# Kernel tuning notes

Hardware: AMD Instinct MI355X
Metric: run time of the kernel (lower is better)

The kernel has to match this reference:

```python
import jax, jax.numpy as jnp
import numpy as np

E = 1024   # embed_dim
H = 16     # num_heads
D = E // H # head dim = 64
L = 1024   # query seq len
S = 1024   # key seq len
N = 4      # batch


def _xavier(key, shape):
    fan_in, fan_out = shape[-1], shape[0]
    if len(shape) == 3:  # attn_W [D, D, H]: torch xavier treats dims (d0, d1*h)
        fan_out, fan_in = shape[0], shape[1] * shape[2]
    scale = jnp.sqrt(6.0 / (fan_in + fan_out)).astype(jnp.float32)
    return jax.random.uniform(key, shape, jnp.float32, -scale, scale)


def setup_inputs() -> dict:
    key = jax.random.key(0)
    ks = jax.random.split(key, 8)
    return {
        "Q": jax.random.normal(ks[0], (L, N, E), jnp.float32),
        "K": jax.random.normal(ks[1], (S, N, E), jnp.float32),
        "V": jax.random.normal(ks[2], (S, N, E), jnp.float32),
        "q_w": _xavier(ks[3], (E, E)),
        "k_w": _xavier(ks[4], (E, E)),
        "v_w": _xavier(ks[5], (E, E)),
        "out_w": _xavier(ks[6], (E, E)),
        "in_bias": jnp.zeros((3, E), jnp.float32),
        "out_bias": jnp.zeros((E,), jnp.float32),
        "attn_W": _xavier(ks[7], (D, D, H)),
    }


def reference(Q, K, V, q_w, k_w, v_w, out_w, in_bias, out_bias, attn_W):
    # in-projections: [l,n,e] x [o,e] -> [l,n,o]
    Qp = jnp.einsum('lni,oi->lno', Q, q_w) + in_bias[0]
    Kp = jnp.einsum('sni,oi->sno', K, k_w) + in_bias[1]
    Vp = jnp.einsum('sni,oi->sno', V, v_w) + in_bias[2]
    # split heads as (head_dim D, num_heads H) -- matches torch .view order
    Qh = Qp.reshape(L, N, D, H)
    Kh = Kp.reshape(S, N, D, H)
    Vh = Vp.reshape(S, N, D, H)
    # 'product' attention: per-head bilinear form q^T W_k k
    scores = jnp.einsum('lnok,oik,snik->lsnk', Qh, attn_W, Kh) / jnp.sqrt(jnp.float32(E))
    W = jax.nn.softmax(scores, axis=1)          # softmax over key dim s
    # dropout p=0.0 -> identity
    O = jnp.einsum('lsnk,snik->lnik', W, Vh).reshape(L, N, E)
    out = O @ out_w + out_bias
    # attention map: sum over heads, reshape [L,S,N] -> [N,L,S] (torch .view semantics = reshape)
    Wmap = W.sum(axis=-1).reshape(-1, L, S) / H
    return out, Wmap
```

## Files before the change

kernel.cpp:

```cpp
#include <hip/hip_runtime.h>
#include <cstdint>

typedef __bf16 bf16x8 __attribute__((ext_vector_type(8)));
typedef float f32x4 __attribute__((ext_vector_type(4)));

static const size_t OFF_QW2BF = 0;
static const size_t OFF_KWBF  = 524288;
static const size_t OFF_VWBF  = 1048576;
static const size_t OFF_OWTBF = 1572864;
static const size_t OFF_QB2   = 2097152;
static const size_t OFF_QWBF  = 2098176;
static const size_t OFF_KHBF  = 4195328;
static const size_t OFF_VTBF  = 6292480;
static const size_t OFF_ST    = 8389632;
static const size_t OFF_OBF   = 8520704;

__device__ inline unsigned short f2bf(float f) {
  union { float f; unsigned u; } v; v.f = f;
  const unsigned r = v.u + 0x7FFFu + ((v.u >> 16) & 1u);
  return (unsigned short)(r >> 16);
}

__global__ __launch_bounds__(256) void k_qw2(const float* __restrict__ qw,
    const float* __restrict__ attnW, const float* __restrict__ bias0,
    unsigned short* __restrict__ qw2, float* __restrict__ qb2) {
  const int b = blockIdx.x;
  const int k = b >> 6, i = b & 63;
  const int tid = threadIdx.x;
  __shared__ float aw[64];
  if (tid < 64) aw[tid] = attnW[(tid * 64 + i) * 16 + k] * 0.03125f;
  __syncthreads();
  for (int j = tid; j < 1024; j += 256) {
    float acc = 0.f;
#pragma unroll 8
    for (int o = 0; o < 64; ++o) acc = fmaf(qw[(o * 16 + k) * 1024 + j], aw[o], acc);
    qw2[(size_t)b * 1024 + j] = f2bf(acc);
  }
  if (tid == 0) {
    float acc = 0.f;
    for (int o = 0; o < 64; ++o) acc = fmaf(bias0[o * 16 + k], aw[o], acc);
    qb2[b] = acc;
  }
}

__global__ __launch_bounds__(256) void k_cvt2(const float* __restrict__ a,
    const float* __restrict__ b, unsigned short* __restrict__ oa,
    unsigned short* __restrict__ ob) {
  const int i = blockIdx.x * 256 + threadIdx.x;
  const float4 va = ((const float4*)a)[i];
  ushort4 ha; ha.x = f2bf(va.x); ha.y = f2bf(va.y); ha.z = f2bf(va.z); ha.w = f2bf(va.w);
  ((ushort4*)oa)[i] = ha;
  const float4 vb = ((const float4*)b)[i];
  ushort4 hb; hb.x = f2bf(vb.x); hb.y = f2bf(vb.y); hb.z = f2bf(vb.z); hb.w = f2bf(vb.w);
  ((ushort4*)ob)[i] = hb;
}

__global__ __launch_bounds__(256) void k_tr(const float* __restrict__ w,
    unsigned short* __restrict__ wt) {
  __shared__ float t[64][65];
  const int j0 = blockIdx.y * 64, o0 = blockIdx.x * 64;
  const int tid = threadIdx.x;
  const int r = tid >> 4, c4 = tid & 15;
#pragma unroll
  for (int q = 0; q < 4; ++q) {
    const int row = r + q * 16;
    const float4 v = *(const float4*)&w[(size_t)(j0 + row) * 1024 + o0 + c4 * 4];
    t[row][c4 * 4 + 0] = v.x; t[row][c4 * 4 + 1] = v.y;
    t[row][c4 * 4 + 2] = v.z; t[row][c4 * 4 + 3] = v.w;
  }
  __syncthreads();
#pragma unroll
  for (int q = 0; q < 4; ++q) {
    const int orow = r + q * 16;
    ushort4 h;
    h.x = f2bf(t[c4 * 4 + 0][orow]); h.y = f2bf(t[c4 * 4 + 1][orow]);
    h.z = f2bf(t[c4 * 4 + 2][orow]); h.w = f2bf(t[c4 * 4 + 3][orow]);
    *(ushort4*)&wt[(size_t)(o0 + orow) * 1024 + j0 + c4 * 4] = h;
  }
}

__global__ __launch_bounds__(256) void k_gemm_in(
    const float* __restrict__ Qf, const float* __restrict__ Kf,
    const float* __restrict__ Vf, const unsigned short* __restrict__ Bq,
    const unsigned short* __restrict__ Bk, const unsigned short* __restrict__ Bv,
    const float* __restrict__ bq, const float* __restrict__ bk,
    const float* __restrict__ bv, unsigned short* __restrict__ Cq,
    unsigned short* __restrict__ Ck, unsigned short* __restrict__ Cv) {
  __shared__ unsigned short As[128][40];
  __shared__ unsigned short Bs[128][40];
  const int id = blockIdx.x;
  const int g  = (id & 7) + ((id >> 6) << 3);
  const int bx = (id >> 3) & 7;
  const int by = g & 31, bz = g >> 5;
  const float* A          = bz == 0 ? Qf : (bz == 1 ? Kf : Vf);
  const unsigned short* B = bz == 0 ? Bq : (bz == 1 ? Bk : Bv);
  const float* bias       = bz == 0 ? bq : (bz == 1 ? bk : bv);
  unsigned short* C       = bz == 0 ? Cq : (bz == 1 ? Ck : Cv);
  const int m0 = by * 128, o0 = bx * 128;
  const int tid = threadIdx.x;
  const int wid = tid >> 6, lane = tid & 63;
  const int wr = wid >> 1, wc = wid & 1;
  const int lr = lane & 15, lk = lane >> 4;
  f32x4 acc[4][4];
#pragma unroll
  for (int i = 0; i < 4; ++i)
#pragma unroll
    for (int j = 0; j < 4; ++j) acc[i][j] = (f32x4){0.f, 0.f, 0.f, 0.f};

  for (int k0 = 0; k0 < 1024; k0 += 32) {
#pragma unroll
    for (int q = 0; q < 4; ++q) {
      const int idx = tid + q * 256;
      const int row = idx >> 3, c4 = idx & 7;
      const float4 v = *(const float4*)&A[(size_t)(m0 + row) * 1024 + k0 + c4 * 4];
      ushort4 h; h.x = f2bf(v.x); h.y = f2bf(v.y); h.z = f2bf(v.z); h.w = f2bf(v.w);
      *(ushort4*)&As[row][c4 * 4] = h;
    }
#pragma unroll
    for (int q = 0; q < 2; ++q) {
      const int idx = tid + q * 256;
      const int row = idx >> 2, c8 = idx & 3;
      *(int4*)&Bs[row][c8 * 8] =
          *(const int4*)&B[(size_t)(o0 + row) * 1024 + k0 + c8 * 8];
    }
    __syncthreads();
    bf16x8 af[4], bfr[4];
#pragma unroll
    for (int f = 0; f < 4; ++f)
      af[f] = *(const bf16x8*)&As[wr * 64 + f * 16 + lr][lk * 8];
#pragma unroll
    for (int f = 0; f < 4; ++f)
      bfr[f] = *(const bf16x8*)&Bs[wc * 64 + f * 16 + lr][lk * 8];
#pragma unroll
    for (int i = 0; i < 4; ++i)
#pragma unroll
      for (int j = 0; j < 4; ++j)
        acc[i][j] = __builtin_amdgcn_mfma_f32_16x16x32_bf16(af[i], bfr[j], acc[i][j], 0, 0, 0);
    __syncthreads();
  }
#pragma unroll
  for (int fi = 0; fi < 4; ++fi)
#pragma unroll
    for (int fj = 0; fj < 4; ++fj) {
      const int o = o0 + wc * 64 + fj * 16 + lr;
      const float bo = bias[o];
#pragma unroll
      for (int t = 0; t < 4; ++t) {
        const int m = m0 + wr * 64 + fi * 16 + lk * 4 + t;
        const float v = acc[fi][fj][t] + bo;
        const int l = m >> 2, nn = m & 3;
        if (bz == 0) {
          const int kk = o >> 6, ii = o & 63;
          C[(((size_t)(nn * 16 + kk) * 1024 + l) << 6) + ii] = f2bf(v);
        } else if (bz == 1) {
          const int kk = o & 15, ii = o >> 4;
          C[(((size_t)(nn * 16 + kk) * 1024 + l) << 6) + ii] = f2bf(v);
        } else {
          const int kk = o & 15, ii = o >> 4;
          C[(((size_t)(nn * 16 + kk) * 64 + ii) << 10) + l] = f2bf(v);
        }
      }
    }
}

__global__ __launch_bounds__(256) void k_gemm_out(
    const unsigned short* __restrict__ A, const unsigned short* __restrict__ B,
    const float* __restrict__ bias, float* __restrict__ C) {
  __shared__ unsigned short As[64][40];
  __shared__ unsigned short Bs[128][40];
  const int id = blockIdx.x;
  const int g  = (id & 7) + ((id >> 6) << 3);
  const int bx = (id >> 3) & 7;
  const int m0 = g * 64, o0 = bx * 128;
  const int tid = threadIdx.x;
  const int wid = tid >> 6, lane = tid & 63;
  const int wr = wid >> 1, wc = wid & 1;
  const int lr = lane & 15, lk = lane >> 4;
  f32x4 acc[2][4];
#pragma unroll
  for (int i = 0; i < 2; ++i)
#pragma unroll
    for (int j = 0; j < 4; ++j) acc[i][j] = (f32x4){0.f, 0.f, 0.f, 0.f};

  for (int k0 = 0; k0 < 1024; k0 += 32) {
    {
      const int row = tid >> 2, c8 = tid & 3;
      *(int4*)&As[row][c8 * 8] =
          *(const int4*)&A[(size_t)(m0 + row) * 1024 + k0 + c8 * 8];
    }
#pragma unroll
    for (int q = 0; q < 2; ++q) {
      const int idx = tid + q * 256;
      const int row = idx >> 2, c8 = idx & 3;
      *(int4*)&Bs[row][c8 * 8] =
          *(const int4*)&B[(size_t)(o0 + row) * 1024 + k0 + c8 * 8];
    }
    __syncthreads();
    bf16x8 af[2], bfr[4];
#pragma unroll
    for (int f = 0; f < 2; ++f)
      af[f] = *(const bf16x8*)&As[wr * 32 + f * 16 + lr][lk * 8];
#pragma unroll
    for (int f = 0; f < 4; ++f)
      bfr[f] = *(const bf16x8*)&Bs[wc * 64 + f * 16 + lr][lk * 8];
#pragma unroll
    for (int i = 0; i < 2; ++i)
#pragma unroll
      for (int j = 0; j < 4; ++j)
        acc[i][j] = __builtin_amdgcn_mfma_f32_16x16x32_bf16(af[i], bfr[j], acc[i][j], 0, 0, 0);
    __syncthreads();
  }
#pragma unroll
  for (int fi = 0; fi < 2; ++fi)
#pragma unroll
    for (int fj = 0; fj < 4; ++fj) {
      const int o = o0 + wc * 64 + fj * 16 + lr;
      const float bo = bias[o];
#pragma unroll
      for (int t = 0; t < 4; ++t) {
        const int m = m0 + wr * 32 + fi * 16 + lk * 4 + t;
        C[(size_t)m * 1024 + o] = acc[fi][fj][t] + bo;
      }
    }
}

__global__ __launch_bounds__(256) void k_flash(
    const unsigned short* __restrict__ Qbf, const unsigned short* __restrict__ Khbf,
    const unsigned short* __restrict__ Vtbf, float* __restrict__ stats,
    unsigned short* __restrict__ Obf) {
  __shared__ unsigned short Kd[2][64 * 64];
  __shared__ unsigned short Vd[2][64 * 64];
  __shared__ unsigned short Ps[4][16 * 64];
  const int ob = blockIdx.x;
  const int b = (ob & 7) * 128 + (ob >> 3);
  const int lt = b & 15, k = (b >> 4) & 15, n = b >> 8;
  const int l0 = lt * 64;
  const int tid = threadIdx.x, w = tid >> 6, lane = tid & 63;
  const int lr = lane & 15, lk = lane >> 4;
  const size_t hb = (size_t)(n * 16 + k) * 65536;
  const unsigned short* qrow = Qbf + hb + (size_t)(l0 + w * 16 + lr) * 64;
  const bf16x8 qa0 = *(const bf16x8*)(qrow + lk * 8);
  const bf16x8 qa1 = *(const bf16x8*)(qrow + 32 + lk * 8);
  const int swz = lr & 7;
  int srow[2], scol[2];
#pragma unroll
  for (int q = 0; q < 2; ++q) {
    const int idx = q * 256 + tid;
    srow[q] = idx >> 3;
    scol[q] = (((idx & 7) ^ ((idx >> 3) & 7)) << 3);
  }
  const unsigned short* Kb = Khbf + hb;
  const unsigned short* Vb = Vtbf + hb;
  int4 kreg[2], vreg[2];
#pragma unroll
  for (int q = 0; q < 2; ++q) {
    kreg[q] = *(const int4*)(Kb + (size_t)srow[q] * 64 + scol[q]);
    vreg[q] = *(const int4*)(Vb + (size_t)srow[q] * 1024 + scol[q]);
  }
#pragma unroll
  for (int q = 0; q < 2; ++q) {
    *(int4*)&Kd[0][(q * 256 + tid) * 8] = kreg[q];
    *(int4*)&Vd[0][(q * 256 + tid) * 8] = vreg[q];
  }
  float m_ = -1e30f, Z_ = 0.f;
  f32x4 oacc[4];
#pragma unroll
  for (int it = 0; it < 4; ++it) oacc[it] = (f32x4){0.f, 0.f, 0.f, 0.f};
  __syncthreads();

  for (int t0 = 0; t0 < 16; ++t0) {
    const int cur = t0 & 1;
    if (t0 < 15) {
      const int s1 = (t0 + 1) * 64;
#pragma unroll
      for (int q = 0; q < 2; ++q) {
        kreg[q] = *(const int4*)(Kb + (size_t)(s1 + srow[q]) * 64 + scol[q]);
        vreg[q] = *(const int4*)(Vb + (size_t)srow[q] * 1024 + s1 + scol[q]);
      }
    }
    f32x4 sc[4];
#pragma unroll
    for (int st = 0; st < 4; ++st) {
      const int r = st * 16 + lr;
      const bf16x8 kb0 = *(const bf16x8*)&Kd[cur][r * 64 + ((lk ^ (r & 7)) << 3)];
      const bf16x8 kb1 = *(const bf16x8*)&Kd[cur][r * 64 + (((4 + lk) ^ (r & 7)) << 3)];
      f32x4 z = (f32x4){0.f, 0.f, 0.f, 0.f};
      z = __builtin_amdgcn_mfma_f32_16x16x32_bf16(kb0, qa0, z, 0, 0, 0);
      sc[st] = __builtin_amdgcn_mfma_f32_16x16x32_bf16(kb1, qa1, z, 0, 0, 0);
    }
    float tm = fmaxf(fmaxf(fmaxf(sc[0][0], sc[0][1]), fmaxf(sc[0][2], sc[0][3])),
                     fmaxf(fmaxf(sc[1][0], sc[1][1]), fmaxf(sc[1][2], sc[1][3])));
    tm = fmaxf(tm, fmaxf(fmaxf(fmaxf(sc[2][0], sc[2][1]), fmaxf(sc[2][2], sc[2][3])),
                         fmaxf(fmaxf(sc[3][0], sc[3][1]), fmaxf(sc[3][2], sc[3][3]))));
    tm = fmaxf(tm, __shfl_xor(tm, 16));
    tm = fmaxf(tm, __shfl_xor(tm, 32));
    const float mn = fmaxf(m_, tm);
    const float fac = __expf(m_ - mn);
    m_ = mn;
    float rs = 0.f;
    float p[4][4];
#pragma unroll
    for (int st = 0; st < 4; ++st)
#pragma unroll
      for (int t = 0; t < 4; ++t) {
        p[st][t] = __expf(sc[st][t] - mn);
        rs += p[st][t];
      }
    rs += __shfl_xor(rs, 16);
    rs += __shfl_xor(rs, 32);
    Z_ = Z_ * fac + rs;
#pragma unroll
    for (int st = 0; st < 4; ++st) {
      ushort4 pk;
      pk.x = f2bf(p[st][0]); pk.y = f2bf(p[st][1]);
      pk.z = f2bf(p[st][2]); pk.w = f2bf(p[st][3]);
      const int c = (st * 4 + lk) ^ (swz << 1);
      *(ushort4*)&Ps[w][lr * 64 + c * 4] = pk;
    }
    float fr[4];
#pragma unroll
    for (int t = 0; t < 4; ++t) fr[t] = __shfl(fac, lk * 4 + t);
    const f32x4 facv = {fr[0], fr[1], fr[2], fr[3]};
    const bf16x8 pa0 = *(const bf16x8*)&Ps[w][lr * 64 + ((lk ^ swz) << 3)];
    const bf16x8 pa1 = *(const bf16x8*)&Ps[w][lr * 64 + (((4 + lk) ^ swz) << 3)];
#pragma unroll
    for (int it = 0; it < 4; ++it) {
      const int r = it * 16 + lr;
      const bf16x8 bv0 = *(const bf16x8*)&Vd[cur][r * 64 + ((lk ^ (r & 7)) << 3)];
      const bf16x8 bv1 = *(const bf16x8*)&Vd[cur][r * 64 + (((4 + lk) ^ (r & 7)) << 3)];
      f32x4 o = oacc[it] * facv;
      o = __builtin_amdgcn_mfma_f32_16x16x32_bf16(pa0, bv0, o, 0, 0, 0);
      oacc[it] = __builtin_amdgcn_mfma_f32_16x16x32_bf16(pa1, bv1, o, 0, 0, 0);
    }
    if (t0 < 15) {
#pragma unroll
      for (int q = 0; q < 2; ++q) {
        *(int4*)&Kd[cur ^ 1][(q * 256 + tid) * 8] = kreg[q];
        *(int4*)&Vd[cur ^ 1][(q * 256 + tid) * 8] = vreg[q];
      }
    }
    __syncthreads();
  }

  if (lane < 16) {
    const size_t so = ((size_t)(n * 16 + k) * 1024 + l0 + w * 16 + lr) * 2;
    stats[so] = m_;
    stats[so + 1] = Z_;
  }
  const float iz = 1.f / Z_;
  float izr[4];
#pragma unroll
  for (int t = 0; t < 4; ++t) izr[t] = __shfl(iz, lk * 4 + t);
#pragma unroll
  for (int it = 0; it < 4; ++it)
#pragma unroll
    for (int t = 0; t < 4; ++t) {
      const int l = l0 + w * 16 + lk * 4 + t;
      const int i = it * 16 + lr;
      Obf[(size_t)(l * 4 + n) * 1024 + i * 16 + k] = f2bf(oacc[it][t] * izr[t]);
    }
}

__global__ __launch_bounds__(256) void k_wmap(const unsigned short* __restrict__ Qbf,
    const unsigned short* __restrict__ Khbf, const float* __restrict__ stats,
    float* __restrict__ Wmap) {
  __shared__ unsigned short Kst[2][64 * 64];
  const int ob = blockIdx.x;
  const int b = (ob & 7) * 128 + (ob >> 3);
  const int st = b & 15, lt = (b >> 4) & 15, n = b >> 8;
  const int l0 = lt * 64, s0 = st * 64;
  const int tid = threadIdx.x, w = tid >> 6, lane = tid & 63;
  const int lr = lane & 15, lk = lane >> 4;
  int srow[2], scol[2];
#pragma unroll
  for (int q = 0; q < 2; ++q) {
    const int idx = q * 256 + tid;
    srow[q] = idx >> 3;
    scol[q] = (((idx & 7) ^ ((idx >> 3) & 7)) << 3);
  }
  int4 kreg[2];
#pragma unroll
  for (int q = 0; q < 2; ++q)
    kreg[q] = *(const int4*)(Khbf + (size_t)(n * 16) * 65536 +
                             (size_t)(s0 + srow[q]) * 64 + scol[q]);
#pragma unroll
  for (int q = 0; q < 2; ++q)
    *(int4*)&Kst[0][(q * 256 + tid) * 8] = kreg[q];
  f32x4 wsum[4];
#pragma unroll
  for (int i = 0; i < 4; ++i) wsum[i] = (f32x4){0.f, 0.f, 0.f, 0.f};
  __syncthreads();

  for (int k = 0; k < 16; ++k) {
    const int cur = k & 1;
    const size_t hb = (size_t)(n * 16 + k) * 65536;
    if (k < 15) {
      const size_t hb1 = (size_t)(n * 16 + k + 1) * 65536;
#pragma unroll
      for (int q = 0; q < 2; ++q)
        kreg[q] = *(const int4*)(Khbf + hb1 + (size_t)(s0 + srow[q]) * 64 + scol[q]);
    }
    const unsigned short* qrow = Qbf + hb + (size_t)(l0 + w * 16 + lr) * 64;
    const bf16x8 a0 = *(const bf16x8*)(qrow + lk * 8);
    const bf16x8 a1 = *(const bf16x8*)(qrow + 32 + lk * 8);
    float mv[4], izv[4];
#pragma unroll
    for (int t = 0; t < 4; ++t) {
      const float2 mz = *(const float2*)(stats +
          ((size_t)(n * 16 + k) * 1024 + l0 + w * 16 + lk * 4 + t) * 2);
      mv[t] = mz.x; izv[t] = 1.f / mz.y;
    }
#pragma unroll
    for (int st2 = 0; st2 < 4; ++st2) {
      const int r = st2 * 16 + lr;
      const bf16x8 kb0 = *(const bf16x8*)&Kst[cur][r * 64 + ((lk ^ (r & 7)) << 3)];
      const bf16x8 kb1 = *(const bf16x8*)&Kst[cur][r * 64 + (((4 + lk) ^ (r & 7)) << 3)];
      f32x4 z = (f32x4){0.f, 0.f, 0.f, 0.f};
      z = __builtin_amdgcn_mfma_f32_16x16x32_bf16(a0, kb0, z, 0, 0, 0);
      z = __builtin_amdgcn_mfma_f32_16x16x32_bf16(a1, kb1, z, 0, 0, 0);
#pragma unroll
      for (int t = 0; t < 4; ++t)
        wsum[st2][t] += __expf(z[t] - mv[t]) * izv[t];
    }
    if (k < 15) {
#pragma unroll
      for (int q = 0; q < 2; ++q)
        *(int4*)&Kst[cur ^ 1][(q * 256 + tid) * 8] = kreg[q];
    }
    __syncthreads();
  }
#pragma unroll
  for (int st2 = 0; st2 < 4; ++st2)
#pragma unroll
    for (int t = 0; t < 4; ++t) {
      const int l = l0 + w * 16 + lk * 4 + t;
      const int s = s0 + st2 * 16 + lr;
      Wmap[((size_t)l * 1024 + s) * 4 + n] = wsum[st2][t] * 0.0625f;
    }
}

extern "C" void kernel_launch(void* const* d_in, const int* in_sizes, int n_in,
                              void* d_out, int out_size, void* d_ws, size_t ws_size,
                              hipStream_t stream) {
  (void)in_sizes; (void)n_in; (void)out_size; (void)ws_size;
  const float* Q        = (const float*)d_in[0];
  const float* K        = (const float*)d_in[1];
  const float* V        = (const float*)d_in[2];
  const float* q_w      = (const float*)d_in[3];
  const float* k_w      = (const float*)d_in[4];
  const float* v_w      = (const float*)d_in[5];
  const float* out_w    = (const float*)d_in[6];
  const float* in_bias  = (const float*)d_in[7];
  const float* out_bias = (const float*)d_in[8];
  const float* attn_W   = (const float*)d_in[9];
  float* ws = (float*)d_ws;
  unsigned short* qw2bf = (unsigned short*)(ws + OFF_QW2BF);
  unsigned short* kwbf  = (unsigned short*)(ws + OFF_KWBF);
  unsigned short* vwbf  = (unsigned short*)(ws + OFF_VWBF);
  unsigned short* owtbf = (unsigned short*)(ws + OFF_OWTBF);
  float* qb2 = ws + OFF_QB2;
  unsigned short* Qwbf = (unsigned short*)(ws + OFF_QWBF);
  unsigned short* Khbf = (unsigned short*)(ws + OFF_KHBF);
  unsigned short* Vtbf = (unsigned short*)(ws + OFF_VTBF);
  float* st = ws + OFF_ST;
  unsigned short* Obf = (unsigned short*)(ws + OFF_OBF);
  float* out  = (float*)d_out;
  float* Wmap = out + 4194304;

  k_qw2<<<1024, 256, 0, stream>>>(q_w, attn_W, in_bias, qw2bf, qb2);
  k_cvt2<<<1024, 256, 0, stream>>>(k_w, v_w, kwbf, vwbf);
  k_tr<<<dim3(16, 16), 256, 0, stream>>>(out_w, owtbf);
  k_gemm_in<<<768, 256, 0, stream>>>(Q, K, V, qw2bf, kwbf, vwbf,
                                     qb2, in_bias + 1024, in_bias + 2048,
                                     Qwbf, Khbf, Vtbf);
  k_flash<<<1024, 256, 0, stream>>>(Qwbf, Khbf, Vtbf, st, Obf);
  k_wmap<<<1024, 256, 0, stream>>>(Qwbf, Khbf, st, Wmap);
  k_gemm_out<<<512, 256, 0, stream>>>(Obf, owtbf, out_bias, out);
}
```

Measured before the change: 199.4 us.

## Pre-convert activations to bf16 and double-buffer GEMM tiles with swizzled LDS

Adds a separate kernel that converts Q, K and V to bf16 once, so the input-projection GEMM loads bf16 directly instead of converting fp32 inside every tile load. Both the input and output GEMMs now use register-prefetched, double-buffered shared memory with an XOR-swizzled layout. This overlaps the global loads with the MFMA work and avoids bank conflicts without padding. The cost is an extra kernel launch plus a full fp32 read and bf16 write of the activations to global memory.

```diff
diff --git a/kernel.cpp b/kernel.cpp
--- a/kernel.cpp
+++ b/kernel.cpp
@@ -14,6 +14,7 @@
 static const size_t OFF_VTBF  = 6292480;
 static const size_t OFF_ST    = 8389632;
 static const size_t OFF_OBF   = 8520704;
+static const size_t OFF_ABF   = 10617856;
 
 __device__ inline unsigned short f2bf(float f) {
   union { float f; unsigned u; } v; v.f = f;
@@ -55,6 +56,22 @@
   ((ushort4*)ob)[i] = hb;
 }
 
+__global__ __launch_bounds__(256) void k_cvtA(const float* __restrict__ Q,
+    const float* __restrict__ K, const float* __restrict__ V,
+    unsigned short* __restrict__ out) {
+  const int b = blockIdx.x;
+  const int m = b >> 10;
+  const float* src = m == 0 ? Q : (m == 1 ? K : V);
+  unsigned short* dst = out + (size_t)m * 4194304;
+#pragma unroll
+  for (int q = 0; q < 4; ++q) {
+    const int idx = (b & 1023) * 1024 + q * 256 + threadIdx.x;
+    const float4 v = ((const float4*)src)[idx];
+    ushort4 h; h.x = f2bf(v.x); h.y = f2bf(v.y); h.z = f2bf(v.z); h.w = f2bf(v.w);
+    ((ushort4*)dst)[idx] = h;
+  }
+}
+
 __global__ __launch_bounds__(256) void k_tr(const float* __restrict__ w,
     unsigned short* __restrict__ wt) {
   __shared__ float t[64][65];
@@ -80,19 +97,18 @@
 }
 
 __global__ __launch_bounds__(256) void k_gemm_in(
-    const float* __restrict__ Qf, const float* __restrict__ Kf,
-    const float* __restrict__ Vf, const unsigned short* __restrict__ Bq,
+    const unsigned short* __restrict__ Abf, const unsigned short* __restrict__ Bq,
     const unsigned short* __restrict__ Bk, const unsigned short* __restrict__ Bv,
     const float* __restrict__ bq, const float* __restrict__ bk,
     const float* __restrict__ bv, unsigned short* __restrict__ Cq,
     unsigned short* __restrict__ Ck, unsigned short* __restrict__ Cv) {
-  __shared__ unsigned short As[128][40];
-  __shared__ unsigned short Bs[128][40];
+  __shared__ unsigned short As[2][128 * 32];
+  __shared__ unsigned short Bs[2][128 * 32];
   const int id = blockIdx.x;
   const int g  = (id & 7) + ((id >> 6) << 3);
   const int bx = (id >> 3) & 7;
   const int by = g & 31, bz = g >> 5;
-  const float* A          = bz == 0 ? Qf : (bz == 1 ? Kf : Vf);
+  const unsigned short* A = Abf + (size_t)bz * 4194304;
   const unsigned short* B = bz == 0 ? Bq : (bz == 1 ? Bk : Bv);
   const float* bias       = bz == 0 ? bq : (bz == 1 ? bk : bv);
   unsigned short* C       = bz == 0 ? Cq : (bz == 1 ? Ck : Cv);
@@ -101,41 +117,64 @@
   const int wid = tid >> 6, lane = tid & 63;
   const int wr = wid >> 1, wc = wid & 1;
   const int lr = lane & 15, lk = lane >> 4;
+  int srow[2], scol[2];
+#pragma unroll
+  for (int q = 0; q < 2; ++q) {
+    const int idx = q * 256 + tid;
+    srow[q] = idx >> 2;
+    scol[q] = (((idx & 3) ^ ((idx >> 2) & 3)) << 3);
+  }
   f32x4 acc[4][4];
 #pragma unroll
   for (int i = 0; i < 4; ++i)
 #pragma unroll
     for (int j = 0; j < 4; ++j) acc[i][j] = (f32x4){0.f, 0.f, 0.f, 0.f};
 
+  int4 areg[2], breg[2];
+#pragma unroll
+  for (int q = 0; q < 2; ++q) {
+    areg[q] = *(const int4*)&A[(size_t)(m0 + srow[q]) * 1024 + scol[q]];
+    breg[q] = *(const int4*)&B[(size_t)(o0 + srow[q]) * 1024 + scol[q]];
+  }
+#pragma unroll
+  for (int q = 0; q < 2; ++q) {
+    *(int4*)&As[0][(q * 256 + tid) * 8] = areg[q];
+    *(int4*)&Bs[0][(q * 256 + tid) * 8] = breg[q];
+  }
+  __syncthreads();
+
   for (int k0 = 0; k0 < 1024; k0 += 32) {
-#pragma unroll
-    for (int q = 0; q < 4; ++q) {
-      const int idx = tid + q * 256;
-      const int row = idx >> 3, c4 = idx & 7;
-      const float4 v = *(const float4*)&A[(size_t)(m0 + row) * 1024 + k0 + c4 * 4];
-      ushort4 h; h.x = f2bf(v.x); h.y = f2bf(v.y); h.z = f2bf(v.z); h.w = f2bf(v.w);
-      *(ushort4*)&As[row][c4 * 4] = h;
-    }
-#pragma unroll
-    for (int q = 0; q < 2; ++q) {
-      const int idx = tid + q * 256;
-      const int row = idx >> 2, c8 = idx & 3;
-      *(int4*)&Bs[row][c8 * 8] =
-          *(const int4*)&B[(size_t)(o0 + row) * 1024 + k0 + c8 * 8];
-    }
-    __syncthreads();
+    const int cur = (k0 >> 5) & 1;
+    if (k0 < 992) {
+#pragma unroll
+      for (int q = 0; q < 2; ++q) {
+        areg[q] = *(const int4*)&A[(size_t)(m0 + srow[q]) * 1024 + k0 + 32 + scol[q]];
+        breg[q] = *(const int4*)&B[(size_t)(o0 + srow[q]) * 1024 + k0 + 32 + scol[q]];
+      }
+    }
     bf16x8 af[4], bfr[4];
 #pragma unroll
-    for (int f = 0; f < 4; ++f)
-      af[f] = *(const bf16x8*)&As[wr * 64 + f * 16 + lr][lk * 8];
-#pragma unroll
-    for (int f = 0; f < 4; ++f)
-      bfr[f] = *(const bf16x8*)&Bs[wc * 64 + f * 16 + lr][lk * 8];
+    for (int f = 0; f < 4; ++f) {
+      const int row = wr * 64 + f * 16 + lr;
+      af[f] = *(const bf16x8*)&As[cur][row * 32 + ((lk ^ (row & 3)) << 3)];
+    }
+#pragma unroll
+    for (int f = 0; f < 4; ++f) {
+      const int row = wc * 64 + f * 16 + lr;
+      bfr[f] = *(const bf16x8*)&Bs[cur][row * 32 + ((lk ^ (row & 3)) << 3)];
+    }
 #pragma unroll
     for (int i = 0; i < 4; ++i)
 #pragma unroll
       for (int j = 0; j < 4; ++j)
         acc[i][j] = __builtin_amdgcn_mfma_f32_16x16x32_bf16(af[i], bfr[j], acc[i][j], 0, 0, 0);
+    if (k0 < 992) {
+#pragma unroll
+      for (int q = 0; q < 2; ++q) {
+        *(int4*)&As[cur ^ 1][(q * 256 + tid) * 8] = areg[q];
+        *(int4*)&Bs[cur ^ 1][(q * 256 + tid) * 8] = breg[q];
+      }
+    }
     __syncthreads();
   }
 #pragma unroll
@@ -166,8 +205,8 @@
 __global__ __launch_bounds__(256) void k_gemm_out(
     const unsigned short* __restrict__ A, const unsigned short* __restrict__ B,
     const float* __restrict__ bias, float* __restrict__ C) {
-  __shared__ unsigned short As[64][40];
-  __shared__ unsigned short Bs[128][40];
+  __shared__ unsigned short As[2][64 * 32];
+  __shared__ unsigned short Bs[2][128 * 32];
   const int id = blockIdx.x;
   const int g  = (id & 7) + ((id >> 6) << 3);
   const int bx = (id >> 3) & 7;
@@ -176,38 +215,61 @@
   const int wid = tid >> 6, lane = tid & 63;
   const int wr = wid >> 1, wc = wid & 1;
   const int lr = lane & 15, lk = lane >> 4;
+  const int sra = tid >> 2, sca = (((tid & 3) ^ ((tid >> 2) & 3)) << 3);
+  int srb[2], scb[2];
+#pragma unroll
+  for (int q = 0; q < 2; ++q) {
+    const int idx = q * 256 + tid;
+    srb[q] = idx >> 2;
+    scb[q] = (((idx & 3) ^ ((idx >> 2) & 3)) << 3);
+  }
   f32x4 acc[2][4];
 #pragma unroll
   for (int i = 0; i < 2; ++i)
 #pragma unroll
     for (int j = 0; j < 4; ++j) acc[i][j] = (f32x4){0.f, 0.f, 0.f, 0.f};
 
+  int4 areg, breg[2];
+  areg = *(const int4*)&A[(size_t)(m0 + sra) * 1024 + sca];
+#pragma unroll
+  for (int q = 0; q < 2; ++q)
+    breg[q] = *(const int4*)&B[(size_t)(o0 + srb[q]) * 1024 + scb[q]];
+  *(int4*)&As[0][tid * 8] = areg;
+#pragma unroll
+  for (int q = 0; q < 2; ++q)
+    *(int4*)&Bs[0][(q * 256 + tid) * 8] = breg[q];
+  __syncthreads();
+
   for (int k0 = 0; k0 < 1024; k0 += 32) {
-    {
-      const int row = tid >> 2, c8 = tid & 3;
-      *(int4*)&As[row][c8 * 8] =
-          *(const int4*)&A[(size_t)(m0 + row) * 1024 + k0 + c8 * 8];
-    }
-#pragma unroll
-    for (int q = 0; q < 2; ++q) {
-      const int idx = tid + q * 256;
-      const int row = idx >> 2, c8 = idx & 3;
-      *(int4*)&Bs[row][c8 * 8] =
-          *(const int4*)&B[(size_t)(o0 + row) * 1024 + k0 + c8 * 8];
-    }
-    __syncthreads();
+    const int cur = (k0 >> 5) & 1;
+    if (k0 < 992) {
+      areg = *(const int4*)&A[(size_t)(m0 + sra) * 1024 + k0 + 32 + sca];
+#pragma unroll
+      for (int q = 0; q < 2; ++q)
+        breg[q] = *(const int4*)&B[(size_t)(o0 + srb[q]) * 1024 + k0 + 32 + scb[q]];
+    }
     bf16x8 af[2], bfr[4];
 #pragma unroll
-    for (int f = 0; f < 2; ++f)
-      af[f] = *(const bf16x8*)&As[wr * 32 + f * 16 + lr][lk * 8];
-#pragma unroll
-    for (int f = 0; f < 4; ++f)
-      bfr[f] = *(const bf16x8*)&Bs[wc * 64 + f * 16 + lr][lk * 8];
+    for (int f = 0; f < 2; ++f) {
+      const int row = wr * 32 + f * 16 + lr;
+      af[f] = *(const bf16x8*)&As[cur][row * 32 + ((lk ^ (row & 3)) << 3)];
+    }
+#pragma unroll
+    for (int f = 0; f < 4; ++f) {
+      const int row = wc * 64 + f * 16 + lr;
+      bfr[f] = *(const bf16x8*)&Bs[cur][row * 32 + ((lk ^ (row & 3)) << 3)];
+    }
 #pragma unroll
     for (int i = 0; i < 2; ++i)
 #pragma unroll
       for (int j = 0; j < 4; ++j)
         acc[i][j] = __builtin_amdgcn_mfma_f32_16x16x32_bf16(af[i], bfr[j], acc[i][j], 0, 0, 0);
+    if (k0 < 992) {
+      *(int4*)&As[cur ^ 1][tid * 8] = areg;
+#pragma unroll
+      for (int q = 0; q < 2; ++q)
+        *(int4*)&Bs[cur ^ 1][(q * 256 + tid) * 8] = breg[q];
+    }
     __syncthreads();
   }
 #pragma unroll
@@ -463,14 +525,16 @@
   unsigned short* Khbf = (unsigned short*)(ws + OFF_KHBF);
   unsigned short* Vtbf = (unsigned short*)(ws + OFF_VTBF);
   float* st = ws + OFF_ST;
-  unsigned short* Obf = (unsigned short*)(ws + OFF_OBF);
+  unsigned short* Obf  = (unsigned short*)(ws + OFF_OBF);
+  unsigned short* Abf  = (unsigned short*)(ws + OFF_ABF);
   float* out  = (float*)d_out;
   float* Wmap = out + 4194304;
 
   k_qw2<<<1024, 256, 0, stream>>>(q_w, attn_W, in_bias, qw2bf, qb2);
   k_cvt2<<<1024, 256, 0, stream>>>(k_w, v_w, kwbf, vwbf);
+  k_cvtA<<<3072, 256, 0, stream>>>(Q, K, V, Abf);
   k_tr<<<dim3(16, 16), 256, 0, stream>>>(out_w, owtbf);
-  k_gemm_in<<<768, 256, 0, stream>>>(Q, K, V, qw2bf, kwbf, vwbf,
+  k_gemm_in<<<768, 256, 0, stream>>>(Abf, qw2bf, kwbf, vwbf,
                                      qb2, in_bias + 1024, in_bias + 2048,
                                      Qwbf, Khbf, Vtbf);
   k_flash<<<1024, 256, 0, stream>>>(Qwbf, Khbf, Vtbf, st, Obf);
```

Measured after the change: 286.4 us. 1.44x slower.
